# Kernel optimization log

Hardware: AMD Instinct MI355X
Metric: run time of the kernel (lower is better)

Reference implementation:

```python
import jax, jax.numpy as jnp
import numpy as np

N, D, E, TOPK = 8192, 2048, 8, 2

def setup_inputs() -> dict:
    key = jax.random.key(0)
    k1, k2, k3, k4 = jax.random.split(key, 4)
    inputs = jax.random.normal(k1, (N, D), dtype=jnp.float32)
    Wg = jax.random.normal(k2, (D, E), dtype=jnp.float32) * 0.02
    We = jax.random.normal(k3, (E, D, D), dtype=jnp.float32) * 0.02
    be = jax.random.normal(k4, (E, D), dtype=jnp.float32) * 0.02
    return {"inputs": inputs, "Wg": Wg, "We": We, "be": be}

def reference(inputs, Wg, We, be):
    # gate: [N, E] logits, top-k routing, softmax over the k selected logits (in fp32)
    gate_logits = inputs @ Wg                      # [N, E]
    topk_vals, selected = jax.lax.top_k(gate_logits, TOPK)  # [N, K], [N, K]
    weights = jax.nn.softmax(topk_vals.astype(jnp.float32), axis=1).astype(inputs.dtype)  # [N, K]

    results = jnp.zeros_like(inputs)
    for i in range(E):
        # combine weight for expert i per token (0 if not routed to i)
        coeff = jnp.sum(jnp.where(selected == i, weights, 0.0), axis=1)  # [N]
        expert_out = inputs @ We[i] + be[i]        # [N, D]
        results = results + coeff[:, None] * expert_out
    return results
```

## Files before the change

kernel.cpp:

```cpp
#include <hip/hip_runtime.h>
#include <stdint.h>

typedef unsigned short u16;
typedef __bf16 bf16x8 __attribute__((ext_vector_type(8)));
typedef float  f32x4  __attribute__((ext_vector_type(4)));

#define N_TOK 8192
#define DIM   2048
#define NEXP  8
#define RPAD  17408

#define OFF_CNT   0
#define OFF_RE    256
#define OFF_RI    (OFF_RE + N_TOK * 8)
#define OFF_RW    (OFF_RI + N_TOK * 16)
#define OFF_TIDX  (OFF_RW + N_TOK * 8)
#define OFF_XB    (OFF_TIDX + NEXP * N_TOK * 4)
#define OFF_WT    (OFF_XB + (size_t)N_TOK * DIM * 2)
#define OFF_YP    (OFF_WT + (size_t)NEXP * DIM * DIM * 2)

__device__ __forceinline__ unsigned f2bf(float f) {
    unsigned int u = __float_as_uint(f);
    u = (u + 0x7FFFu + ((u >> 16) & 1u)) >> 16;
    return u;
}

__device__ __forceinline__ void gload16(const void* g, void* l) {
    __builtin_amdgcn_global_load_lds(
        (const __attribute__((address_space(1))) unsigned int*)g,
        (__attribute__((address_space(3))) unsigned int*)l,
        16, 0, 0);
}

__global__ __launch_bounds__(256) void k_gate(
    const float* __restrict__ x, const float* __restrict__ Wg,
    int2* __restrict__ route_e, float2* __restrict__ route_w,
    u16* __restrict__ Xb) {
    int wave = threadIdx.x >> 6, lane = threadIdx.x & 63;
    int n = blockIdx.x * 4 + wave;
    const float* xr = x + (size_t)n * DIM;
    u16* xbr = Xb + (size_t)n * DIM;
    double acc[8] = {0, 0, 0, 0, 0, 0, 0, 0};
#pragma unroll
    for (int it = 0; it < 4; it++) {
        int c = it * 512 + lane * 8;
        float4 a = *(const float4*)(xr + c);
        float4 b = *(const float4*)(xr + c + 4);
        uint4 o;
        o.x = f2bf(a.x) | (f2bf(a.y) << 16);
        o.y = f2bf(a.z) | (f2bf(a.w) << 16);
        o.z = f2bf(b.x) | (f2bf(b.y) << 16);
        o.w = f2bf(b.z) | (f2bf(b.w) << 16);
        *(uint4*)(xbr + c) = o;
        float xv[8] = {a.x, a.y, a.z, a.w, b.x, b.y, b.z, b.w};
        const float4* wp = (const float4*)(Wg + (size_t)c * 8);
#pragma unroll
        for (int j = 0; j < 8; j++) {
            float4 w0 = wp[j * 2], w1 = wp[j * 2 + 1];
            double xd = (double)xv[j];
            acc[0] += xd * (double)w0.x;
            acc[1] += xd * (double)w0.y;
            acc[2] += xd * (double)w0.z;
            acc[3] += xd * (double)w0.w;
            acc[4] += xd * (double)w1.x;
            acc[5] += xd * (double)w1.y;
            acc[6] += xd * (double)w1.z;
            acc[7] += xd * (double)w1.w;
        }
    }
#pragma unroll
    for (int off = 32; off; off >>= 1)
#pragma unroll
        for (int e = 0; e < 8; e++) acc[e] += __shfl_xor(acc[e], off);
    if (lane == 0) {
        float v[8];
#pragma unroll
        for (int e = 0; e < 8; e++) v[e] = (float)acc[e];
        int e0 = 0; float v0 = v[0];
#pragma unroll
        for (int e = 1; e < 8; e++) if (v[e] > v0) { v0 = v[e]; e0 = e; }
        int e1 = -1; float v1 = -1e30f;
#pragma unroll
        for (int e = 0; e < 8; e++) if (e != e0 && v[e] > v1) { v1 = v[e]; e1 = e; }
        float ex = expf(v1 - v0);
        route_e[n] = make_int2(e0, e1);
        route_w[n] = make_float2(1.0f / (1.0f + ex), ex / (1.0f + ex));
    }
}

__global__ __launch_bounds__(256) void k_slots(
    const int2* __restrict__ route_e, int4* __restrict__ route_i,
    int* __restrict__ cnt, int* __restrict__ tok_idx) {
    __shared__ int lc[256][NEXP];
    int t = threadIdx.x;
#pragma unroll
    for (int e = 0; e < NEXP; e++) lc[t][e] = 0;
    int2 re[32];
#pragma unroll 4
    for (int i = 0; i < 32; i++) {
        re[i] = route_e[t * 32 + i];
        lc[t][re[i].x]++;
        lc[t][re[i].y]++;
    }
    __syncthreads();
    if (t < NEXP) {
        int run = 0;
        for (int b = 0; b < 256; b++) { int v = lc[b][t]; lc[b][t] = run; run += v; }
        cnt[t] = run;
    }
    __syncthreads();
#pragma unroll 4
    for (int i = 0; i < 32; i++) {
        int n = t * 32 + i;
        int p0 = lc[t][re[i].x]++;
        int p1 = lc[t][re[i].y]++;
        route_i[n] = make_int4(re[i].x, re[i].y, p0, p1);
        tok_idx[re[i].x * N_TOK + p0] = n;
        tok_idx[re[i].y * N_TOK + p1] = n;
    }
}

__global__ void k_transpose_we(const float* __restrict__ We, u16* __restrict__ Wt) {
    __shared__ float t[64][65];
    int e = blockIdx.z, k0 = blockIdx.y * 64, n0 = blockIdx.x * 64;
    const float* src = We + ((size_t)e * DIM + k0) * DIM + n0;
    int tid = threadIdx.x;
#pragma unroll
    for (int it = 0; it < 4; it++) {
        int item = it * 256 + tid;
        int r = item >> 4, c4 = (item & 15) * 4;
        float4 v = *(const float4*)(src + (size_t)r * DIM + c4);
        t[r][c4] = v.x; t[r][c4 + 1] = v.y; t[r][c4 + 2] = v.z; t[r][c4 + 3] = v.w;
    }
    __syncthreads();
    u16* dst = Wt + ((size_t)e * DIM + n0) * DIM + k0;
#pragma unroll
    for (int it = 0; it < 2; it++) {
        int item = it * 256 + tid;
        int nl = item >> 3, kc = (item & 7) * 8;
        unsigned m[8];
#pragma unroll
        for (int j = 0; j < 8; j++) m[j] = f2bf(t[kc + j][nl]);
        uint4 o;
        o.x = m[0] | (m[1] << 16); o.y = m[2] | (m[3] << 16);
        o.z = m[4] | (m[5] << 16); o.w = m[6] | (m[7] << 16);
        *(uint4*)(dst + (size_t)nl * DIM + kc) = o;
    }
}

__global__ __launch_bounds__(256) void k_moe_gemm(
    const u16* __restrict__ Xb, const u16* __restrict__ Wt,
    const float* __restrict__ be, const int* __restrict__ cnt,
    const int* __restrict__ tok_idx, u16* __restrict__ Yp) {
    int base[NEXP]; int pb = 0;
#pragma unroll
    for (int i = 0; i < NEXP; i++) { base[i] = pb; pb += ((cnt[i] + 127) >> 7) << 7; }
    int m0 = blockIdx.y * 128;
    if (m0 >= pb) return;
    int e = 0;
#pragma unroll
    for (int i = 1; i < NEXP; i++) if (m0 >= base[i]) e = i;
    int n0 = blockIdx.x * 128;

    __shared__ u16 As[128 * 32];
    __shared__ u16 Bs[128 * 32];

    int tid = threadIdx.x;
    int wave = tid >> 6, lane = tid & 63;

    int srow = wave * 16 + (lane >> 2);
    int scol = ((lane & 3) ^ ((srow >> 1) & 3)) * 8;
    int slot = m0 + srow - base[e];
    int t0 = tok_idx[e * N_TOK + slot] & (N_TOK - 1);
    int t1 = tok_idx[e * N_TOK + slot + 64] & (N_TOK - 1);
    const u16* gA0 = Xb + (size_t)t0 * DIM + scol;
    const u16* gA1 = Xb + (size_t)t1 * DIM + scol;
    const u16* gB0 = Wt + ((size_t)e * DIM + n0 + srow) * DIM + scol;
    const u16* gB1 = gB0 + (size_t)64 * DIM;
    u16* lA0 = As + (wave * 16) * 32;
    u16* lA1 = As + (64 + wave * 16) * 32;
    u16* lB0 = Bs + (wave * 16) * 32;
    u16* lB1 = Bs + (64 + wave * 16) * 32;

    int wr = (wave >> 1) * 64, wc = (wave & 1) * 64;
    int q = lane >> 4, mr = lane & 15;

    f32x4 acc[4][4] = {};

    for (int kk = 0; kk < DIM; kk += 32) {
        gload16(gA0 + kk, lA0);
        gload16(gA1 + kk, lA1);
        gload16(gB0 + kk, lB0);
        gload16(gB1 + kk, lB1);
        __syncthreads();
        bf16x8 af[4], bfr[4];
#pragma unroll
        for (int i = 0; i < 4; i++) {
            int R = wr + i * 16 + mr;
            af[i] = *(const bf16x8*)(As + R * 32 + (q ^ ((R >> 1) & 3)) * 8);
        }
#pragma unroll
        for (int j = 0; j < 4; j++) {
            int R = wc + j * 16 + mr;
            bfr[j] = *(const bf16x8*)(Bs + R * 32 + (q ^ ((R >> 1) & 3)) * 8);
        }
#pragma unroll
        for (int i = 0; i < 4; i++)
#pragma unroll
            for (int j = 0; j < 4; j++)
                acc[i][j] = __builtin_amdgcn_mfma_f32_16x16x32_bf16(
                    af[i], bfr[j], acc[i][j], 0, 0, 0);
        __syncthreads();
    }

    float bev[4];
#pragma unroll
    for (int j = 0; j < 4; j++) bev[j] = be[e * DIM + n0 + wc + j * 16 + mr];
#pragma unroll
    for (int i = 0; i < 4; i++) {
#pragma unroll
        for (int r = 0; r < 4; r++) {
            int row = wr + i * 16 + q * 4 + r;
            u16* yrow = Yp + (size_t)(m0 + row) * DIM + n0 + wc + mr;
#pragma unroll
            for (int j = 0; j < 4; j++)
                yrow[j * 16] = (u16)f2bf(acc[i][j][r] + bev[j]);
        }
    }
}

__global__ __launch_bounds__(256) void k_combine(
    const u16* __restrict__ Yp, const int* __restrict__ cnt,
    const int4* __restrict__ route_i, const float2* __restrict__ route_w,
    float* __restrict__ out) {
    int base[NEXP]; int pb = 0;
#pragma unroll
    for (int i = 0; i < NEXP; i++) { base[i] = pb; pb += ((cnt[i] + 127) >> 7) << 7; }
    int n = blockIdx.x, tid = threadIdx.x;
    int4 ri = route_i[n]; float2 w = route_w[n];
    size_t r0 = (size_t)base[ri.x] + ri.z;
    size_t r1 = (size_t)base[ri.y] + ri.w;
    uint4 ya = ((const uint4*)(Yp + r0 * DIM))[tid];
    uint4 yb = ((const uint4*)(Yp + r1 * DIM))[tid];
    float4 o0, o1;
    unsigned a, b;
    a = ya.x; b = yb.x;
    o0.x = w.x * __uint_as_float(a << 16) + w.y * __uint_as_float(b << 16);
    o0.y = w.x * __uint_as_float(a & 0xffff0000u) + w.y * __uint_as_float(b & 0xffff0000u);
    a = ya.y; b = yb.y;
    o0.z = w.x * __uint_as_float(a << 16) + w.y * __uint_as_float(b << 16);
    o0.w = w.x * __uint_as_float(a & 0xffff0000u) + w.y * __uint_as_float(b & 0xffff0000u);
    a = ya.z; b = yb.z;
    o1.x = w.x * __uint_as_float(a << 16) + w.y * __uint_as_float(b << 16);
    o1.y = w.x * __uint_as_float(a & 0xffff0000u) + w.y * __uint_as_float(b & 0xffff0000u);
    a = ya.w; b = yb.w;
    o1.z = w.x * __uint_as_float(a << 16) + w.y * __uint_as_float(b << 16);
    o1.w = w.x * __uint_as_float(a & 0xffff0000u) + w.y * __uint_as_float(b & 0xffff0000u);
    float4* op = (float4*)(out + (size_t)n * DIM) + tid * 2;
    op[0] = o0; op[1] = o1;
}

extern "C" void kernel_launch(void* const* d_in, const int* in_sizes, int n_in,
                              void* d_out, int out_size, void* d_ws, size_t ws_size,
                              hipStream_t stream) {
    const float* x  = (const float*)d_in[0];
    const float* Wg = (const float*)d_in[1];
    const float* We = (const float*)d_in[2];
    const float* be = (const float*)d_in[3];
    float* out = (float*)d_out;
    char* ws = (char*)d_ws;
    int*    cnt     = (int*)(ws + OFF_CNT);
    int2*   route_e = (int2*)(ws + OFF_RE);
    int4*   route_i = (int4*)(ws + OFF_RI);
    float2* route_w = (float2*)(ws + OFF_RW);
    int*    tok_idx = (int*)(ws + OFF_TIDX);
    u16*    Xb      = (u16*)(ws + OFF_XB);
    u16*    Wt      = (u16*)(ws + OFF_WT);
    u16*    Yp      = (u16*)(ws + OFF_YP);

    k_gate<<<N_TOK / 4, 256, 0, stream>>>(x, Wg, route_e, route_w, Xb);
    k_slots<<<1, 256, 0, stream>>>(route_e, route_i, cnt, tok_idx);
    k_transpose_we<<<dim3(DIM / 64, DIM / 64, NEXP), 256, 0, stream>>>(We, Wt);
    k_moe_gemm<<<dim3(DIM / 128, RPAD / 128, 1), 256, 0, stream>>>(
        Xb, Wt, be, cnt, tok_idx, Yp);
    k_combine<<<N_TOK, 256, 0, stream>>>(Yp, cnt, route_i, route_w, out);
}
```

Measured before the change: 540.7 us.

## Parallelize routing slot assignment and coarsen expert weight transpose blocks

Replaces the single-block serial slot-assignment kernel with three kernels: a per-chunk histogram over 32 blocks, a tiny prefix scan, and a ballot/popcount ranking pass that computes stable per-expert positions in parallel. Separately, each transpose block now handles four 64-row K tiles in a loop, cutting the block count by a factor of four. The aim is to remove the latency of the one-block serial routing kernel, at the cost of two extra kernel launches. The slot ordering within an expert changes: token-major order is kept for the first choice, but second-choice slots now come after all first-choice slots in each chunk.

```diff
diff --git a/kernel.cpp b/kernel.cpp
--- a/kernel.cpp
+++ b/kernel.cpp
@@ -9,9 +9,12 @@
 #define DIM   2048
 #define NEXP  8
 #define RPAD  17408
+#define NCHUNK 32
 
 #define OFF_CNT   0
-#define OFF_RE    256
+#define OFF_HIST  1024
+#define OFF_PRE   2048
+#define OFF_RE    4096
 #define OFF_RI    (OFF_RE + N_TOK * 8)
 #define OFF_RW    (OFF_RI + N_TOK * 16)
 #define OFF_TIDX  (OFF_RW + N_TOK * 8)
@@ -88,63 +91,90 @@
     }
 }
 
-__global__ __launch_bounds__(256) void k_slots(
-    const int2* __restrict__ route_e, int4* __restrict__ route_i,
-    int* __restrict__ cnt, int* __restrict__ tok_idx) {
-    __shared__ int lc[256][NEXP];
-    int t = threadIdx.x;
-#pragma unroll
-    for (int e = 0; e < NEXP; e++) lc[t][e] = 0;
-    int2 re[32];
-#pragma unroll 4
-    for (int i = 0; i < 32; i++) {
-        re[i] = route_e[t * 32 + i];
-        lc[t][re[i].x]++;
-        lc[t][re[i].y]++;
-    }
+__global__ __launch_bounds__(256) void k_hist(
+    const int2* __restrict__ route_e, int* __restrict__ hist) {
+    __shared__ int h[NEXP];
+    int c = blockIdx.x, t = threadIdx.x;
+    if (t < NEXP) h[t] = 0;
     __syncthreads();
-    if (t < NEXP) {
+    int2 re = route_e[c * 256 + t];
+    atomicAdd(&h[re.x], 1);
+    atomicAdd(&h[re.y], 1);
+    __syncthreads();
+    if (t < NEXP) hist[c * NEXP + t] = h[t];
+}
+
+__global__ void k_scan(const int* __restrict__ hist, int* __restrict__ pre,
+                       int* __restrict__ cnt) {
+    int e = threadIdx.x;
+    if (e < NEXP) {
         int run = 0;
-        for (int b = 0; b < 256; b++) { int v = lc[b][t]; lc[b][t] = run; run += v; }
-        cnt[t] = run;
+        for (int c = 0; c < NCHUNK; c++) { pre[c * NEXP + e] = run; run += hist[c * NEXP + e]; }
+        cnt[e] = run;
+    }
+}
+
+__global__ __launch_bounds__(256) void k_assign(
+    const int2* __restrict__ route_e, const int* __restrict__ pre,
+    int4* __restrict__ route_i, int* __restrict__ tok_idx) {
+    __shared__ int wc0[4][NEXP], wc1[4][NEXP];
+    int c = blockIdx.x, t = threadIdx.x, wave = t >> 6, lane = t & 63;
+    int n = c * 256 + t;
+    int2 re = route_e[n];
+    unsigned long long lt = ((unsigned long long)1 << lane) - 1;
+    int r0 = 0, r1 = 0;
+#pragma unroll
+    for (int e = 0; e < NEXP; e++) {
+        unsigned long long m0 = __ballot(re.x == e);
+        unsigned long long m1 = __ballot(re.y == e);
+        if (lane == 0) { wc0[wave][e] = __popcll(m0); wc1[wave][e] = __popcll(m1); }
+        if (re.x == e) r0 = __popcll(m0 & lt);
+        if (re.y == e) r1 = __popcll(m1 & lt);
     }
     __syncthreads();
-#pragma unroll 4
-    for (int i = 0; i < 32; i++) {
-        int n = t * 32 + i;
-        int p0 = lc[t][re[i].x]++;
-        int p1 = lc[t][re[i].y]++;
-        route_i[n] = make_int4(re[i].x, re[i].y, p0, p1);
-        tok_idx[re[i].x * N_TOK + p0] = n;
-        tok_idx[re[i].y * N_TOK + p1] = n;
-    }
-}
-
-__global__ void k_transpose_we(const float* __restrict__ We, u16* __restrict__ Wt) {
+    int h0tot = 0;
+#pragma unroll
+    for (int w = 0; w < 4; w++) {
+        if (w < wave) { r0 += wc0[w][re.x]; r1 += wc1[w][re.y]; }
+        h0tot += wc0[w][re.y];
+    }
+    int p0 = pre[c * NEXP + re.x] + r0;
+    int p1 = pre[c * NEXP + re.y] + h0tot + r1;
+    route_i[n] = make_int4(re.x, re.y, p0, p1);
+    tok_idx[re.x * N_TOK + p0] = n;
+    tok_idx[re.y * N_TOK + p1] = n;
+}
+
+__global__ __launch_bounds__(256) void k_transpose_we(
+    const float* __restrict__ We, u16* __restrict__ Wt) {
     __shared__ float t[64][65];
-    int e = blockIdx.z, k0 = blockIdx.y * 64, n0 = blockIdx.x * 64;
-    const float* src = We + ((size_t)e * DIM + k0) * DIM + n0;
+    int e = blockIdx.z, n0 = blockIdx.x * 64, k00 = blockIdx.y * 256;
     int tid = threadIdx.x;
-#pragma unroll
-    for (int it = 0; it < 4; it++) {
-        int item = it * 256 + tid;
-        int r = item >> 4, c4 = (item & 15) * 4;
-        float4 v = *(const float4*)(src + (size_t)r * DIM + c4);
-        t[r][c4] = v.x; t[r][c4 + 1] = v.y; t[r][c4 + 2] = v.z; t[r][c4 + 3] = v.w;
-    }
-    __syncthreads();
-    u16* dst = Wt + ((size_t)e * DIM + n0) * DIM + k0;
-#pragma unroll
-    for (int it = 0; it < 2; it++) {
-        int item = it * 256 + tid;
-        int nl = item >> 3, kc = (item & 7) * 8;
-        unsigned m[8];
-#pragma unroll
-        for (int j = 0; j < 8; j++) m[j] = f2bf(t[kc + j][nl]);
-        uint4 o;
-        o.x = m[0] | (m[1] << 16); o.y = m[2] | (m[3] << 16);
-        o.z = m[4] | (m[5] << 16); o.w = m[6] | (m[7] << 16);
-        *(uint4*)(dst + (size_t)nl * DIM + kc) = o;
+    for (int kt = 0; kt < 4; kt++) {
+        int k0 = k00 + kt * 64;
+        const float* src = We + ((size_t)e * DIM + k0) * DIM + n0;
+        if (kt) __syncthreads();
+#pragma unroll
+        for (int it = 0; it < 4; it++) {
+            int item = it * 256 + tid;
+            int r = item >> 4, c4 = (item & 15) * 4;
+            float4 v = *(const float4*)(src + (size_t)r * DIM + c4);
+            t[r][c4] = v.x; t[r][c4 + 1] = v.y; t[r][c4 + 2] = v.z; t[r][c4 + 3] = v.w;
+        }
+        __syncthreads();
+        u16* dst = Wt + ((size_t)e * DIM + n0) * DIM + k0;
+#pragma unroll
+        for (int it = 0; it < 2; it++) {
+            int item = it * 256 + tid;
+            int nl = item >> 3, kc = (item & 7) * 8;
+            unsigned m[8];
+#pragma unroll
+            for (int j = 0; j < 8; j++) m[j] = f2bf(t[kc + j][nl]);
+            uint4 o;
+            o.x = m[0] | (m[1] << 16); o.y = m[2] | (m[3] << 16);
+            o.z = m[4] | (m[5] << 16); o.w = m[6] | (m[7] << 16);
+            *(uint4*)(dst + (size_t)nl * DIM + kc) = o;
+        }
     }
 }
 
@@ -270,6 +300,8 @@
     float* out = (float*)d_out;
     char* ws = (char*)d_ws;
     int*    cnt     = (int*)(ws + OFF_CNT);
+    int*    hist    = (int*)(ws + OFF_HIST);
+    int*    pre     = (int*)(ws + OFF_PRE);
     int2*   route_e = (int2*)(ws + OFF_RE);
     int4*   route_i = (int4*)(ws + OFF_RI);
     float2* route_w = (float2*)(ws + OFF_RW);
@@ -279,8 +311,10 @@
     u16*    Yp      = (u16*)(ws + OFF_YP);
 
     k_gate<<<N_TOK / 4, 256, 0, stream>>>(x, Wg, route_e, route_w, Xb);
-    k_slots<<<1, 256, 0, stream>>>(route_e, route_i, cnt, tok_idx);
-    k_transpose_we<<<dim3(DIM / 64, DIM / 64, NEXP), 256, 0, stream>>>(We, Wt);
+    k_hist<<<NCHUNK, 256, 0, stream>>>(route_e, hist);
+    k_scan<<<1, 64, 0, stream>>>(hist, pre, cnt);
+    k_assign<<<NCHUNK, 256, 0, stream>>>(route_e, pre, route_i, tok_idx);
+    k_transpose_we<<<dim3(DIM / 64, DIM / 256, NEXP), 256, 0, stream>>>(We, Wt);
     k_moe_gemm<<<dim3(DIM / 128, RPAD / 128, 1), 256, 0, stream>>>(
         Xb, Wt, be, cnt, tok_idx, Yp);
     k_combine<<<N_TOK, 256, 0, stream>>>(Yp, cnt, route_i, route_w, out);
```

New measurement: 515.3 us. 4.7% less time.
